# Performance work log

Hardware: AMD Instinct MI355X
Metric: run time of the kernel (lower is better)

The kernel has to match this reference:

```python
import jax, jax.numpy as jnp
import numpy as np
from jax import lax

# Key identity used: modulating ALL weights of output channel o by s_o (with no bias
# inside the modulated conv, as in the source where F.conv2d(..., bias=None)) is
# mathematically identical to a plain conv followed by per-(batch, out_channel)
# scaling of the output. This collapses the per-sample Python loop into one conv.

def _upsample2x(x):
    # nearest-neighbor x2, matching F.interpolate(scale_factor=2) default mode
    return jnp.repeat(jnp.repeat(x, 2, axis=2), 2, axis=3)

def _conv(x, w):
    return lax.conv_general_dilated(
        x, w, window_strides=(1, 1), padding=[(1, 1), (1, 1)],
        dimension_numbers=("NCHW", "OIHW", "NCHW"))

def _modconv(x, style, w, fc_w, fc_b):
    # style_fc: [B, style_dim] -> [B, out_ch]
    s = style @ fc_w.T + fc_b          # [B, O]
    y = _conv(x, w)                    # [B, O, H, W]
    return y * s[:, :, None, None]


def setup_inputs() -> dict:
    key = jax.random.key(0)
    ks = jax.random.split(key, 16)
    B, SD = 8, 512
    chans = [(512, 256), (256, 128), (128, 64), (64, 64), (64, 64)]
    inp = {
        "x": jax.random.normal(ks[0], (B, 512, 8, 8), jnp.float32),
        "style": jax.random.normal(ks[1], (B, SD), jnp.float32),
    }
    for i, (ci, co) in enumerate(chans, start=1):
        inp[f"w{i}"] = jax.random.normal(ks[2 * i], (co, ci, 3, 3), jnp.float32) * (1.0 / np.sqrt(ci * 9))
        inp[f"fw{i}"] = jax.random.normal(ks[2 * i + 1], (co, SD), jnp.float32) * (1.0 / np.sqrt(SD))
        inp[f"fb{i}"] = jnp.ones((co,), jnp.float32)
    inp["wf"] = jax.random.normal(ks[12], (3, 64, 3, 3), jnp.float32) * (1.0 / np.sqrt(64 * 9))
    inp["bf"] = jnp.zeros((3,), jnp.float32)
    return inp


def reference(x, style, w1, fw1, fb1, w2, fw2, fb2, w3, fw3, fb3,
              w4, fw4, fb4, w5, fw5, fb5, wf, bf):
    x = _upsample2x(x)
    x = jax.nn.relu(_modconv(x, style, w1, fw1, fb1))
    x = _upsample2x(x)
    x = jax.nn.relu(_modconv(x, style, w2, fw2, fb2))
    x = _upsample2x(x)
    x = jax.nn.relu(_modconv(x, style, w3, fw3, fb3))
    x = _upsample2x(x)
    x = jax.nn.relu(_modconv(x, style, w4, fw4, fb4))
    x = _upsample2x(x)
    x = jax.nn.relu(_modconv(x, style, w5, fw5, fb5))
    x = _conv(x, wf) + bf[None, :, None, None]
    return x
```

## Files before the change

kernel.cpp:

```cpp
#include <hip/hip_runtime.h>
#include <hip/hip_bf16.h>
#include <cstddef>

typedef __bf16 bf16x8 __attribute__((ext_vector_type(8)));
typedef float f32x4 __attribute__((ext_vector_type(4)));


__global__ void convert_x_kernel(const float* __restrict__ x, __hip_bfloat16* __restrict__ act0) {
    int t = blockIdx.x * 256 + threadIdx.x;
    int c = t & 511; int rest = t >> 9;
    int w = rest & 7; rest >>= 3; int h = rest & 7; int b = rest >> 3;
    act0[t] = __float2bfloat16(x[((b * 512 + c) * 8 + h) * 8 + w]);
}

__global__ void wtrans_all_kernel(const float* __restrict__ w1, __hip_bfloat16* __restrict__ o1,
                                  const float* __restrict__ w2, __hip_bfloat16* __restrict__ o2,
                                  const float* __restrict__ w3, __hip_bfloat16* __restrict__ o3,
                                  const float* __restrict__ w4, __hip_bfloat16* __restrict__ o4,
                                  const float* __restrict__ w5, __hip_bfloat16* __restrict__ o5,
                                  const float* __restrict__ wf, __hip_bfloat16* __restrict__ of) {
    int t = blockIdx.x * 256 + threadIdx.x;
    if (t >= 1631232) return;
    if (t < 1548288) {
        const float* w; __hip_bfloat16* o; int lgci, lgco;
        if      (t < 1179648) { w = w1; o = o1; lgci = 9; lgco = 8; }
        else if (t < 1474560) { t -= 1179648; w = w2; o = o2; lgci = 8; lgco = 7; }
        else                  { t -= 1474560; w = w3; o = o3; lgci = 7; lgco = 6; }
        int CI = 1 << lgci;
        int ci = t & (CI - 1);
        int co = (t >> lgci) & ((1 << lgco) - 1);
        int tap = t >> (lgci + lgco);
        o[t] = __float2bfloat16(w[((size_t)co * CI + ci) * 9 + tap]);
    } else if (t < 1622016) {
        const float* w; __hip_bfloat16* o;
        if (t < 1585152) { t -= 1548288; w = w4; o = o4; }
        else             { t -= 1585152; w = w5; o = o5; }
        int j  = t & 7;
        int ln = (t >> 3) & 63;
        int ch = (t >> 9) & 1;
        int nt = (t >> 10) & 3;
        int tap = t >> 12;
        int rr = ln & 15, qq = ln >> 4;
        int co = nt * 16 + rr;
        int ci = ch * 32 + qq * 8 + j;
        o[t] = __float2bfloat16(w[((size_t)co * 64 + ci) * 9 + tap]);
    } else {
        int u = t - 1622016;
        int j  = u & 7;
        int ln = (u >> 3) & 63;
        int ch = (u >> 9) & 1;
        int tap = u >> 10;
        int rr = ln & 15, qq = ln >> 4;
        int ci = ch * 32 + qq * 8 + j;
        float v = (rr < 3) ? wf[((size_t)rr * 64 + ci) * 9 + tap] : 0.f;
        of[u] = __float2bfloat16(v);
    }
}

__global__ void style_all_kernel(const float* __restrict__ style,
                                 const float* __restrict__ fw1, const float* __restrict__ fb1,
                                 const float* __restrict__ fw2, const float* __restrict__ fb2,
                                 const float* __restrict__ fw3, const float* __restrict__ fb3,
                                 const float* __restrict__ fw4, const float* __restrict__ fb4,
                                 const float* __restrict__ fw5, const float* __restrict__ fb5,
                                 float* __restrict__ S) {
    int wvid = blockIdx.x * 4 + (threadIdx.x >> 6);
    int lane = threadIdx.x & 63;
    const float* fw; const float* fb; int lg, sOff, local;
    if      (wvid < 2048) { fw = fw1; fb = fb1; lg = 8; sOff = 0;    local = wvid; }
    else if (wvid < 3072) { fw = fw2; fb = fb2; lg = 7; sOff = 2048; local = wvid - 2048; }
    else if (wvid < 3584) { fw = fw3; fb = fb3; lg = 6; sOff = 3072; local = wvid - 3072; }
    else if (wvid < 4096) { fw = fw4; fb = fb4; lg = 6; sOff = 3584; local = wvid - 3584; }
    else                  { fw = fw5; fb = fb5; lg = 6; sOff = 4096; local = wvid - 4096; }
    int b = local >> lg, o = local & ((1 << lg) - 1);
    const float* sb = style + b * 512;
    const float* fwo = fw + (size_t)o * 512;
    float p = 0.f;
    #pragma unroll
    for (int k = lane; k < 512; k += 64) p += sb[k] * fwo[k];
    #pragma unroll
    for (int off = 32; off > 0; off >>= 1) p += __shfl_down(p, off);
    if (lane == 0) S[sOff + local] = p + fb[o];
}

template <int CI, int CO, int HS, int WS>
__launch_bounds__(512)
__global__ void conv_partial_kernel(const __hip_bfloat16* __restrict__ actIn,
                                    const __hip_bfloat16* __restrict__ wtr,
                                    float* __restrict__ Part) {
    constexpr int HO = HS * 2, WO = WS * 2;
    constexpr size_t sliceN = (size_t)8 * HO * WO * CO;
    const int tid = threadIdx.x;
    const int lane = tid & 63, wv = tid >> 6;
    const int r = lane & 15, q = lane >> 4;
    const int pw = WO / 16, ppb = (HO / 16) * pw;
    const int b = blockIdx.x / ppb;
    const int prest = blockIdx.x - b * ppb;
    const int ph = prest / pw, pwi = prest - ph * pw;
    const int oh0 = ph * 16, ow0 = pwi * 16;
    const int sh0 = oh0 >> 1, sw0 = ow0 >> 1;
    const int n0 = blockIdx.y * 64;
    const int ciOff = blockIdx.z * 64;

    __shared__ alignas(16) __hip_bfloat16 Tile[100 * 72];
    __shared__ alignas(16) __hip_bfloat16 Wlds[2][64 * 72];

    f32x4 acc[2][4];
    #pragma unroll
    for (int i = 0; i < 2; ++i)
        #pragma unroll
        for (int j = 0; j < 4; ++j) acc[i][j] = f32x4{0.f, 0.f, 0.f, 0.f};

    for (int i = tid; i < 800; i += 512) {
        int pix = i >> 3, koct = i & 7;
        int tr = pix / 10, tc2 = pix - tr * 10;
        int su = sh0 - 1 + tr, sv = sw0 - 1 + tc2;
        uint4 v = {0, 0, 0, 0};
        if (su >= 0 && su < HS && sv >= 0 && sv < WS)
            v = *(const uint4*)(actIn + ((size_t)((b * HS + su) * WS + sv) * CI + ciOff + koct * 8));
        *(uint4*)&Tile[pix * 72 + koct * 8] = v;
    }
    {
        int co = tid >> 3, koct = tid & 7;
        *(uint4*)&Wlds[0][co * 72 + koct * 8] =
            *(const uint4*)(wtr + ((size_t)(n0 + co)) * CI + ciOff + koct * 8);
    }
    __syncthreads();

    #pragma unroll 1
    for (int tap = 0; tap < 9; ++tap) {
        const bool pf = (tap < 8);
        uint4 wr0 = {0,0,0,0};
        if (pf) {
            int co0 = tid >> 3, k0 = tid & 7;
            wr0 = *(const uint4*)(wtr + ((size_t)(tap + 1) * CO + n0 + co0) * CI + ciOff + k0 * 8);
        }
        const int dyv = tap / 3;
        const int dxm1 = tap - dyv * 3 - 1;
        const int tc = ((r + dxm1) >> 1) + 1;
        int apix[2];
        #pragma unroll
        for (int mt = 0; mt < 2; ++mt)
            apix[mt] = ((((wv * 2 + mt) + dyv - 1) >> 1) + 1) * 10 + tc;

        const int buf = tap & 1;
        #pragma unroll
        for (int ch = 0; ch < 2; ++ch) {
            bf16x8 af[2], bfr[4];
            #pragma unroll
            for (int mt = 0; mt < 2; ++mt)
                af[mt] = *(const bf16x8*)&Tile[apix[mt] * 72 + ch * 32 + q * 8];
            #pragma unroll
            for (int nt = 0; nt < 4; ++nt)
                bfr[nt] = *(const bf16x8*)&Wlds[buf][(nt * 16 + r) * 72 + ch * 32 + q * 8];
            #pragma unroll
            for (int mt = 0; mt < 2; ++mt)
                #pragma unroll
                for (int nt = 0; nt < 4; ++nt)
                    acc[mt][nt] = __builtin_amdgcn_mfma_f32_16x16x32_bf16(
                        af[mt], bfr[nt], acc[mt][nt], 0, 0, 0);
        }
        if (pf) {
            int nb = buf ^ 1;
            int co0 = tid >> 3, k0 = tid & 7;
            *(uint4*)&Wlds[nb][co0 * 72 + k0 * 8] = wr0;
            __syncthreads();
        }
    }

    float* P = Part + (size_t)blockIdx.z * sliceN;
    #pragma unroll
    for (int mt = 0; mt < 2; ++mt) {
        const int prow = wv * 2 + mt;
        #pragma unroll
        for (int t2 = 0; t2 < 4; ++t2) {
            const int pcol = q * 4 + t2;
            const size_t obase = ((size_t)(b * HO + oh0 + prow) * WO + ow0 + pcol) * CO + n0;
            #pragma unroll
            for (int nt = 0; nt < 4; ++nt)
                P[obase + nt * 16 + r] = acc[mt][nt][t2];
        }
    }
}

template <int KS, int CO, int HW>
__launch_bounds__(256)
__global__ void reduce_kernel(const float* __restrict__ Part, const float* __restrict__ S,
                              __hip_bfloat16* __restrict__ actOut) {
    constexpr size_t sliceN = (size_t)8 * HW * CO;
    size_t e = ((size_t)blockIdx.x * 256 + threadIdx.x) * 4;
    if (e >= sliceN) return;
    f32x4 sum = {0.f, 0.f, 0.f, 0.f};
    #pragma unroll
    for (int k = 0; k < KS; ++k) sum += *(const f32x4*)(Part + (size_t)k * sliceN + e);
    const int co = (int)(e & (CO - 1));
    const int b = (int)(e / ((size_t)HW * CO));
    const float* Sb = S + b * CO + co;
    union { ushort4 u; __hip_bfloat16 h[4]; } pack;
    #pragma unroll
    for (int j = 0; j < 4; ++j)
        pack.h[j] = __float2bfloat16(fmaxf(sum[j] * Sb[j], 0.f));
    *(ushort4*)((unsigned short*)actOut + e) = pack.u;
}

template <int HS, int WS>
__launch_bounds__(256)
__global__ void conv_patch_kernel(const __hip_bfloat16* __restrict__ actIn,
                                  const __hip_bfloat16* __restrict__ wpk,
                                  const float* __restrict__ S,
                                  __hip_bfloat16* __restrict__ actOut) {
    constexpr int HO = HS * 2, WO = WS * 2;

    const int tid = threadIdx.x;
    const int lane = tid & 63, wv = tid >> 6;
    const int r = lane & 15, q = lane >> 4;
    const int lane8 = lane * 8;

    const int pw = WO / 16, ppb = (HO / 16) * pw;
    const int b = blockIdx.x / ppb;
    const int prest = blockIdx.x - b * ppb;
    const int ph = prest / pw, pwi = prest - ph * pw;
    const int oh0 = ph * 16, ow0 = pwi * 16;
    const int sh0 = oh0 >> 1, sw0 = ow0 >> 1;
    const int by = blockIdx.y;
    const int n0 = by * 32;

    __shared__ alignas(16) __hip_bfloat16 Tile[100 * 72];

    f32x4 acc[4][2];
    #pragma unroll
    for (int i = 0; i < 4; ++i)
        #pragma unroll
        for (int j = 0; j < 2; ++j) acc[i][j] = f32x4{0.f, 0.f, 0.f, 0.f};

    const int wv4 = wv * 4;

    for (int i = tid; i < 800; i += 256) {
        int pix = i >> 3, koct = i & 7;
        int tr = pix / 10, tc2 = pix - tr * 10;
        int su = sh0 - 1 + tr, sv = sw0 - 1 + tc2;
        uint4 v = {0, 0, 0, 0};
        if (su >= 0 && su < HS && sv >= 0 && sv < WS)
            v = *(const uint4*)(actIn + ((size_t)((b * HS + su) * WS + sv) * 64 + koct * 8));
        *(uint4*)&Tile[pix * 72 + koct * 8] = v;
    }
    __syncthreads();

    bf16x8 bA[2][2], bB[2][2];

    auto loadB = [&](bf16x8 (&dst)[2][2], int tap) {
        #pragma unroll
        for (int nt = 0; nt < 2; ++nt)
            #pragma unroll
            for (int ch = 0; ch < 2; ++ch)
                dst[nt][ch] = *(const bf16x8*)(
                    wpk + ((tap * 8 + (by * 2 + nt) * 2 + ch) << 9) + lane8);
    };

    auto compute = [&](int tap, bf16x8 (&bfr)[2][2]) {
        const int dyv = tap / 3;
        const int dxm1 = tap - dyv * 3 - 1;
        const int tc = ((r + dxm1) >> 1) + 1;
        int apix[4];
        #pragma unroll
        for (int mt = 0; mt < 4; ++mt)
            apix[mt] = ((((wv4 + mt) + dyv - 1) >> 1) + 1) * 10 + tc;
        #pragma unroll
        for (int ch = 0; ch < 2; ++ch) {
            bf16x8 af[4];
            #pragma unroll
            for (int mt = 0; mt < 4; ++mt)
                af[mt] = *(const bf16x8*)&Tile[apix[mt] * 72 + ch * 32 + q * 8];
            #pragma unroll
            for (int mt = 0; mt < 4; ++mt)
                #pragma unroll
                for (int nt = 0; nt < 2; ++nt)
                    acc[mt][nt] = __builtin_amdgcn_mfma_f32_16x16x32_bf16(
                        af[mt], bfr[nt][ch], acc[mt][nt], 0, 0, 0);
        }
    };

    loadB(bA, 0);
    #pragma unroll 1
    for (int it = 0; it < 4; ++it) {
        loadB(bB, 2 * it + 1);
        compute(2 * it, bA);
        loadB(bA, 2 * it + 2);
        compute(2 * it + 1, bB);
    }
    compute(8, bA);

    float sv_[2];
    #pragma unroll
    for (int nt = 0; nt < 2; ++nt) sv_[nt] = S[b * 64 + n0 + nt * 16 + r];
    #pragma unroll
    for (int mt = 0; mt < 4; ++mt) {
        const int prow = wv4 + mt;
        #pragma unroll
        for (int t2 = 0; t2 < 4; ++t2) {
            const int pcol = q * 4 + t2;
            const size_t obase = ((size_t)(b * HO + oh0 + prow) * WO + ow0 + pcol) * 64 + n0;
            #pragma unroll
            for (int nt = 0; nt < 2; ++nt)
                actOut[obase + nt * 16 + r] =
                    __float2bfloat16(fmaxf(acc[mt][nt][t2] * sv_[nt], 0.f));
        }
    }
}

__launch_bounds__(256)
__global__ void conv_final_kernel(const __hip_bfloat16* __restrict__ actIn,
                                  const __hip_bfloat16* __restrict__ wpkF,
                                  const float* __restrict__ bias,
                                  float* __restrict__ out) {
    constexpr int HO = 256, WO = 256;
    const int tid = threadIdx.x, lane = tid & 63, wv = tid >> 6;
    const int r = lane & 15, q = lane >> 4;
    const int lane8 = lane * 8;

    const int ppb = 32 * 16;
    const int b = blockIdx.x / ppb;
    const int prest = blockIdx.x - b * ppb;
    const int ph = prest >> 4, pwi = prest & 15;
    const int oh0 = ph * 8, ow0 = pwi * 16;

    __shared__ alignas(16) __hip_bfloat16 Tile[10 * 18 * 72];

    for (int i = tid; i < 1440; i += 256) {
        int pix = i >> 3, koct = i & 7;
        int tr = pix / 18, tc2 = pix - tr * 18;
        int u = oh0 - 1 + tr, v = ow0 - 1 + tc2;
        uint4 val = {0, 0, 0, 0};
        if (u >= 0 && u < HO && v >= 0 && v < WO)
            val = *(const uint4*)(actIn + ((size_t)((b * HO + u) * WO + v) * 64 + koct * 8));
        *(uint4*)&Tile[pix * 72 + koct * 8] = val;
    }
    __syncthreads();

    f32x4 acc[2];
    acc[0] = f32x4{0.f, 0.f, 0.f, 0.f};
    acc[1] = f32x4{0.f, 0.f, 0.f, 0.f};

    #pragma unroll 1
    for (int tap = 0; tap < 9; ++tap) {
        const int dyv = tap / 3;
        const int dxv = tap - dyv * 3;
        const int tc = r + dxv;
        int apix[2];
        #pragma unroll
        for (int mt = 0; mt < 2; ++mt)
            apix[mt] = (wv * 2 + mt + dyv) * 18 + tc;
        #pragma unroll
        for (int ch = 0; ch < 2; ++ch) {
            bf16x8 bfr = *(const bf16x8*)(wpkF + ((tap * 2 + ch) << 9) + lane8);
            #pragma unroll
            for (int mt = 0; mt < 2; ++mt) {
                bf16x8 af = *(const bf16x8*)&Tile[apix[mt] * 72 + ch * 32 + q * 8];
                acc[mt] = __builtin_amdgcn_mfma_f32_16x16x32_bf16(af, bfr, acc[mt], 0, 0, 0);
            }
        }
    }

    if (r < 3) {
        const float bs = bias[r];
        #pragma unroll
        for (int mt = 0; mt < 2; ++mt) {
            const int prow = wv * 2 + mt;
            #pragma unroll
            for (int t2 = 0; t2 < 4; ++t2) {
                const int pcol = q * 4 + t2;
                out[((size_t)(b * 3 + r) << 16) + (oh0 + prow) * 256 + ow0 + pcol] =
                    acc[mt][t2] + bs;
            }
        }
    }
}

extern "C" void kernel_launch(void* const* d_in, const int* in_sizes, int n_in,
                              void* d_out, int out_size, void* d_ws, size_t ws_size,
                              hipStream_t stream) {
    const float* x    = (const float*)d_in[0];
    const float* sty  = (const float*)d_in[1];
    const float* w1   = (const float*)d_in[2];
    const float* fw1  = (const float*)d_in[3];
    const float* fb1  = (const float*)d_in[4];
    const float* w2   = (const float*)d_in[5];
    const float* fw2  = (const float*)d_in[6];
    const float* fb2  = (const float*)d_in[7];
    const float* w3   = (const float*)d_in[8];
    const float* fw3  = (const float*)d_in[9];
    const float* fb3  = (const float*)d_in[10];
    const float* w4   = (const float*)d_in[11];
    const float* fw4  = (const float*)d_in[12];
    const float* fb4  = (const float*)d_in[13];
    const float* w5   = (const float*)d_in[14];
    const float* fw5  = (const float*)d_in[15];
    const float* fb5  = (const float*)d_in[16];
    const float* wf   = (const float*)d_in[17];
    const float* bf   = (const float*)d_in[18];
    float* out = (float*)d_out;

    char* ws = (char*)d_ws;
    size_t off = 0;
    auto alloc = [&](size_t bytes) {
        char* p = ws + off;
        off += (bytes + 255) & ~(size_t)255;
        return p;
    };
    float* S1 = (float*)alloc(8 * 256 * 4);
    float* S2 = (float*)alloc(8 * 128 * 4);
    float* S3 = (float*)alloc(8 * 64 * 4);
    float* S4 = (float*)alloc(8 * 64 * 4);
    float* S5 = (float*)alloc(8 * 64 * 4);
    __hip_bfloat16* act0 = (__hip_bfloat16*)alloc((size_t)262144 * 2);
    __hip_bfloat16* act1 = (__hip_bfloat16*)alloc((size_t)524288 * 2);
    __hip_bfloat16* act2 = (__hip_bfloat16*)alloc((size_t)1048576 * 2);
    __hip_bfloat16* act3 = (__hip_bfloat16*)alloc((size_t)2097152 * 2);
    __hip_bfloat16* act4 = (__hip_bfloat16*)alloc((size_t)8388608 * 2);
    __hip_bfloat16* act5 = (__hip_bfloat16*)alloc((size_t)33554432 * 2);
    __hip_bfloat16* wt1  = (__hip_bfloat16*)alloc((size_t)9 * 256 * 512 * 2);
    __hip_bfloat16* wt2  = (__hip_bfloat16*)alloc((size_t)9 * 128 * 256 * 2);
    __hip_bfloat16* wt3  = (__hip_bfloat16*)alloc((size_t)9 * 64 * 128 * 2);
    __hip_bfloat16* wt4  = (__hip_bfloat16*)alloc((size_t)9 * 64 * 64 * 2);
    __hip_bfloat16* wt5  = (__hip_bfloat16*)alloc((size_t)9 * 64 * 64 * 2);
    __hip_bfloat16* wtF  = (__hip_bfloat16*)alloc((size_t)9 * 16 * 64 * 2);
    if (off > ws_size) return;

    float* Part = (float*)act5;

    convert_x_kernel<<<1024, 256, 0, stream>>>(x, act0);
    wtrans_all_kernel<<<6372, 256, 0, stream>>>(w1, wt1, w2, wt2, w3, wt3,
                                                w4, wt4, w5, wt5, wf, wtF);
    style_all_kernel<<<1152, 256, 0, stream>>>(sty, fw1, fb1, fw2, fb2, fw3, fb3,
                                               fw4, fb4, fw5, fb5, S1);

    conv_partial_kernel<512, 256, 8, 8><<<dim3(8, 4, 8), 512, 0, stream>>>(act0, wt1, Part);
    reduce_kernel<8, 256, 256><<<512, 256, 0, stream>>>(Part, S1, act1);
    conv_partial_kernel<256, 128, 16, 16><<<dim3(32, 2, 4), 512, 0, stream>>>(act1, wt2, Part);
    reduce_kernel<4, 128, 1024><<<1024, 256, 0, stream>>>(Part, S2, act2);
    conv_partial_kernel<128, 64, 32, 32><<<dim3(128, 1, 2), 512, 0, stream>>>(act2, wt3, Part);
    reduce_kernel<2, 64, 4096><<<2048, 256, 0, stream>>>(Part, S3, act3);

    conv_patch_kernel<64, 64><<<dim3(512, 2), 256, 0, stream>>>(act3, wt4, S4, act4);
    conv_patch_kernel<128, 128><<<dim3(2048, 2), 256, 0, stream>>>(act4, wt5, S5, act5);
    conv_final_kernel<<<4096, 256, 0, stream>>>(act5, wtF, bf, out);
}
```

Before: 229.1 us.

## Fold nearest upsample into conv via per-phase 2x2 collapsed weights

Layers 4 and 5, which convolve a nearest-upsampled input, now use precomputed per-output-phase 2x2 kernels made by summing the 3x3 weights that land on the same source pixel. Each wave handles one of the four output phases across all 64 output channels, so the block covers all channels and the grid-y split goes away. This cuts MFMA work from 9 taps to 4 per output and halves the blocks. In exchange it needs more accumulator registers, larger weight fragments per wave, and a heavier weight-prep kernel.

```diff
diff --git a/kernel.cpp b/kernel.cpp
--- a/kernel.cpp
+++ b/kernel.cpp
@@ -20,7 +20,7 @@
                                   const float* __restrict__ w5, __hip_bfloat16* __restrict__ o5,
                                   const float* __restrict__ wf, __hip_bfloat16* __restrict__ of) {
     int t = blockIdx.x * 256 + threadIdx.x;
-    if (t >= 1631232) return;
+    if (t >= 1688576) return;
     if (t < 1548288) {
         const float* w; __hip_bfloat16* o; int lgci, lgco;
         if      (t < 1179648) { w = w1; o = o1; lgci = 9; lgco = 8; }
@@ -31,21 +31,31 @@
         int co = (t >> lgci) & ((1 << lgco) - 1);
         int tap = t >> (lgci + lgco);
         o[t] = __float2bfloat16(w[((size_t)co * CI + ci) * 9 + tap]);
-    } else if (t < 1622016) {
+    } else if (t < 1679360) {
+        int u = t - 1548288;
         const float* w; __hip_bfloat16* o;
-        if (t < 1585152) { t -= 1548288; w = w4; o = o4; }
-        else             { t -= 1585152; w = w5; o = o5; }
-        int j  = t & 7;
-        int ln = (t >> 3) & 63;
-        int ch = (t >> 9) & 1;
-        int nt = (t >> 10) & 3;
-        int tap = t >> 12;
-        int rr = ln & 15, qq = ln >> 4;
-        int co = nt * 16 + rr;
-        int ci = ch * 32 + qq * 8 + j;
-        o[t] = __float2bfloat16(w[((size_t)co * 64 + ci) * 9 + tap]);
+        if (u < 65536) { w = w4; o = o4; }
+        else           { u -= 65536; w = w5; o = o5; }
+        int j   = u & 7;
+        int ln  = (u >> 3) & 63;
+        int ch  = (u >> 9) & 1;
+        int nt  = (u >> 10) & 3;
+        int tp  = (u >> 12) & 3;
+        int cls = (u >> 14) & 3;
+        int py = cls >> 1, px = cls & 1;
+        int i = tp >> 1, jj = tp & 1;
+        int co = nt * 16 + (ln & 15);
+        int ci = ch * 32 + (ln >> 4) * 8 + j;
+        int r0 = i * (1 + py), rc = py ? (2 - i) : (1 + i);
+        int c0 = jj * (1 + px), cc = px ? (2 - jj) : (1 + jj);
+        const float* wb = w + ((size_t)co * 64 + ci) * 9;
+        float s = 0.f;
+        for (int rr = 0; rr < rc; ++rr)
+            for (int c2 = 0; c2 < cc; ++c2)
+                s += wb[(r0 + rr) * 3 + (c0 + c2)];
+        o[u] = __float2bfloat16(s);
     } else {
-        int u = t - 1622016;
+        int u = t - 1679360;
         int j  = u & 7;
         int ln = (u >> 3) & 63;
         int ch = (u >> 9) & 1;
@@ -214,7 +224,9 @@
     const int tid = threadIdx.x;
     const int lane = tid & 63, wv = tid >> 6;
     const int r = lane & 15, q = lane >> 4;
+    const int rs = r >> 3, sc = r & 7;
     const int lane8 = lane * 8;
+    const int py = wv >> 1, px = wv & 1;
 
     const int pw = WO / 16, ppb = (HO / 16) * pw;
     const int b = blockIdx.x / ppb;
@@ -222,18 +234,14 @@
     const int ph = prest / pw, pwi = prest - ph * pw;
     const int oh0 = ph * 16, ow0 = pwi * 16;
     const int sh0 = oh0 >> 1, sw0 = ow0 >> 1;
-    const int by = blockIdx.y;
-    const int n0 = by * 32;
 
     __shared__ alignas(16) __hip_bfloat16 Tile[100 * 72];
 
-    f32x4 acc[4][2];
+    f32x4 acc[4][4];
     #pragma unroll
     for (int i = 0; i < 4; ++i)
         #pragma unroll
-        for (int j = 0; j < 2; ++j) acc[i][j] = f32x4{0.f, 0.f, 0.f, 0.f};
-
-    const int wv4 = wv * 4;
+        for (int j = 0; j < 4; ++j) acc[i][j] = f32x4{0.f, 0.f, 0.f, 0.f};
 
     for (int i = tid; i < 800; i += 256) {
         int pix = i >> 3, koct = i & 7;
@@ -246,25 +254,25 @@
     }
     __syncthreads();
 
-    bf16x8 bA[2][2], bB[2][2];
-
-    auto loadB = [&](bf16x8 (&dst)[2][2], int tap) {
-        #pragma unroll
-        for (int nt = 0; nt < 2; ++nt)
+    const __hip_bfloat16* wcls = wpk + ((size_t)wv << 14);
+
+    bf16x8 bA[4][2], bB[4][2];
+
+    auto loadB = [&](bf16x8 (&dst)[4][2], int tp) {
+        #pragma unroll
+        for (int nt = 0; nt < 4; ++nt)
             #pragma unroll
             for (int ch = 0; ch < 2; ++ch)
-                dst[nt][ch] = *(const bf16x8*)(
-                    wpk + ((tap * 8 + (by * 2 + nt) * 2 + ch) << 9) + lane8);
+                dst[nt][ch] = *(const bf16x8*)(wcls + (tp << 12) + ((nt * 2 + ch) << 9) + lane8);
     };
 
-    auto compute = [&](int tap, bf16x8 (&bfr)[2][2]) {
-        const int dyv = tap / 3;
-        const int dxm1 = tap - dyv * 3 - 1;
-        const int tc = ((r + dxm1) >> 1) + 1;
+    auto compute = [&](int tp, bf16x8 (&bfr)[4][2]) {
+        const int i = tp >> 1, j = tp & 1;
+        const int ro = i + py, co2 = j + px;
         int apix[4];
         #pragma unroll
         for (int mt = 0; mt < 4; ++mt)
-            apix[mt] = ((((wv4 + mt) + dyv - 1) >> 1) + 1) * 10 + tc;
+            apix[mt] = (2 * mt + rs + ro) * 10 + (sc + co2);
         #pragma unroll
         for (int ch = 0; ch < 2; ++ch) {
             bf16x8 af[4];
@@ -274,34 +282,34 @@
             #pragma unroll
             for (int mt = 0; mt < 4; ++mt)
                 #pragma unroll
-                for (int nt = 0; nt < 2; ++nt)
+                for (int nt = 0; nt < 4; ++nt)
                     acc[mt][nt] = __builtin_amdgcn_mfma_f32_16x16x32_bf16(
                         af[mt], bfr[nt][ch], acc[mt][nt], 0, 0, 0);
         }
     };
 
     loadB(bA, 0);
-    #pragma unroll 1
-    for (int it = 0; it < 4; ++it) {
-        loadB(bB, 2 * it + 1);
-        compute(2 * it, bA);
-        loadB(bA, 2 * it + 2);
-        compute(2 * it + 1, bB);
-    }
-    compute(8, bA);
-
-    float sv_[2];
-    #pragma unroll
-    for (int nt = 0; nt < 2; ++nt) sv_[nt] = S[b * 64 + n0 + nt * 16 + r];
+    loadB(bB, 1);
+    compute(0, bA);
+    loadB(bA, 2);
+    compute(1, bB);
+    loadB(bB, 3);
+    compute(2, bA);
+    compute(3, bB);
+
+    float sv_[4];
+    #pragma unroll
+    for (int nt = 0; nt < 4; ++nt) sv_[nt] = S[b * 64 + nt * 16 + r];
     #pragma unroll
     for (int mt = 0; mt < 4; ++mt) {
-        const int prow = wv4 + mt;
         #pragma unroll
         for (int t2 = 0; t2 < 4; ++t2) {
-            const int pcol = q * 4 + t2;
-            const size_t obase = ((size_t)(b * HO + oh0 + prow) * WO + ow0 + pcol) * 64 + n0;
-            #pragma unroll
-            for (int nt = 0; nt < 2; ++nt)
+            const int m = q * 4 + t2;
+            const int row = oh0 + 4 * mt + 2 * (m >> 3) + py;
+            const int col = ow0 + 2 * (m & 7) + px;
+            const size_t obase = ((size_t)(b * HO + row) * WO + col) * 64;
+            #pragma unroll
+            for (int nt = 0; nt < 4; ++nt)
                 actOut[obase + nt * 16 + r] =
                     __float2bfloat16(fmaxf(acc[mt][nt][t2] * sv_[nt], 0.f));
         }
@@ -421,15 +429,15 @@
     __hip_bfloat16* wt1  = (__hip_bfloat16*)alloc((size_t)9 * 256 * 512 * 2);
     __hip_bfloat16* wt2  = (__hip_bfloat16*)alloc((size_t)9 * 128 * 256 * 2);
     __hip_bfloat16* wt3  = (__hip_bfloat16*)alloc((size_t)9 * 64 * 128 * 2);
-    __hip_bfloat16* wt4  = (__hip_bfloat16*)alloc((size_t)9 * 64 * 64 * 2);
-    __hip_bfloat16* wt5  = (__hip_bfloat16*)alloc((size_t)9 * 64 * 64 * 2);
+    __hip_bfloat16* wt4  = (__hip_bfloat16*)alloc((size_t)65536 * 2);
+    __hip_bfloat16* wt5  = (__hip_bfloat16*)alloc((size_t)65536 * 2);
     __hip_bfloat16* wtF  = (__hip_bfloat16*)alloc((size_t)9 * 16 * 64 * 2);
     if (off > ws_size) return;
 
     float* Part = (float*)act5;
 
     convert_x_kernel<<<1024, 256, 0, stream>>>(x, act0);
-    wtrans_all_kernel<<<6372, 256, 0, stream>>>(w1, wt1, w2, wt2, w3, wt3,
+    wtrans_all_kernel<<<6596, 256, 0, stream>>>(w1, wt1, w2, wt2, w3, wt3,
                                                 w4, wt4, w5, wt5, wf, wtF);
     style_all_kernel<<<1152, 256, 0, stream>>>(sty, fw1, fb1, fw2, fb2, fw3, fb3,
                                                fw4, fb4, fw5, fb5, S1);
@@ -441,7 +449,7 @@
     conv_partial_kernel<128, 64, 32, 32><<<dim3(128, 1, 2), 512, 0, stream>>>(act2, wt3, Part);
     reduce_kernel<2, 64, 4096><<<2048, 256, 0, stream>>>(Part, S3, act3);
 
-    conv_patch_kernel<64, 64><<<dim3(512, 2), 256, 0, stream>>>(act3, wt4, S4, act4);
-    conv_patch_kernel<128, 128><<<dim3(2048, 2), 256, 0, stream>>>(act4, wt5, S5, act5);
+    conv_patch_kernel<64, 64><<<dim3(512), 256, 0, stream>>>(act3, wt4, S4, act4);
+    conv_patch_kernel<128, 128><<<dim3(2048), 256, 0, stream>>>(act4, wt5, S5, act5);
     conv_final_kernel<<<4096, 256, 0, stream>>>(act5, wtF, bf, out);
 }
```

Result: faster. 217.4 us (-5.1%).
